# Kernel tuning notes

Measured on AMD Instinct MI355X. Metric: run time of the kernel, lower is better.

Reference implementation:

```python
import jax, jax.numpy as jnp
import numpy as np

B, N, H, P, R = 16, 256, 768, 2048, 3


def setup_inputs() -> dict:
    key = jax.random.key(0)
    ks = jax.random.split(key, 7)
    s_h = 1.0 / np.sqrt(H)
    s_p = 1.0 / np.sqrt(P)
    return {
        "features": jax.random.normal(ks[0], (B, N, H), dtype=jnp.float32),
        "head_W": jax.random.uniform(ks[1], (P, H), jnp.float32, -s_h, s_h),
        "head_b": jax.random.uniform(ks[2], (P,), jnp.float32, -s_h, s_h),
        "tail_W": jax.random.uniform(ks[3], (P, H), jnp.float32, -s_h, s_h),
        "tail_b": jax.random.uniform(ks[4], (P,), jnp.float32, -s_h, s_h),
        "bil_W": jax.random.uniform(ks[5], (R, P, P), jnp.float32, -s_p, s_p),
        "bil_b": jax.random.uniform(ks[6], (R,), jnp.float32, -s_p, s_p),
    }


def reference(features, head_W, head_b, tail_W, tail_b, bil_W, bil_b):
    # Linear projections (dropout is identity in eval mode)
    head = jnp.einsum("bnh,ph->bnp", features, head_W) + head_b  # [B,N,P]
    tail = jnp.einsum("bnh,ph->bnp", features, tail_W) + tail_b  # [B,N,P]
    # Bilinear over all region pairs, without materializing [B,N,N,P]:
    # first contract head with W[r] -> [B,N,R,P], then with tail -> [B,N,N,R]
    hw = jnp.einsum("bnp,rpq->bnrq", head, bil_W)                # [B,N,R,P]
    logits = jnp.einsum("bnrq,bmq->bnmr", hw, tail) + bil_b      # [B,N,N,R]
    return logits
```

## Files before the change

### kernel.cpp

```cpp
#include <hip/hip_runtime.h>

constexpr int Bb = 16;
constexpr int Nn = 256;
constexpr int Hh = 768;
constexpr int Pp = 2048;
constexpr int Rr = 3;
constexpr int Mm = Bb * Nn;
constexpr int HA = 896;
constexpr int KA = 2080;
constexpr int JA = Rr * HA;

typedef __bf16 bf16_t;
typedef __bf16 bf16x8 __attribute__((ext_vector_type(8)));
typedef __bf16 bf16x4 __attribute__((ext_vector_type(4)));
typedef float  floatx4 __attribute__((ext_vector_type(4)));

__device__ __forceinline__ void gld_lds16(const void* g, void* l) {
    __builtin_amdgcn_global_load_lds(
        (__attribute__((address_space(1))) void*)g,
        (__attribute__((address_space(3))) void*)l,
        16, 0, 0);
}

__global__ __launch_bounds__(256) void cvt_bilW(
    const float* __restrict__ in, bf16_t* __restrict__ out)
{
    const size_t i = (size_t)blockIdx.x * 256 + threadIdx.x;
    const float4 v0 = ((const float4*)in)[2 * i];
    const float4 v1 = ((const float4*)in)[2 * i + 1];
    bf16x8 o = { (bf16_t)v0.x, (bf16_t)v0.y, (bf16_t)v0.z, (bf16_t)v0.w,
                 (bf16_t)v1.x, (bf16_t)v1.y, (bf16_t)v1.z, (bf16_t)v1.w };
    ((bf16x8*)out)[i] = o;
}

__global__ __launch_bounds__(256) void build_Faug(
    const float* __restrict__ F, bf16_t* __restrict__ out)
{
    const int idx = blockIdx.x * 256 + threadIdx.x;
    const int n = idx / (HA / 4), c4 = idx % (HA / 4);
    const int h = c4 * 4;
    bf16x4 o;
    if (h < Hh) {
        float4 v = *(const float4*)(F + (size_t)n * Hh + h);
        o = { (bf16_t)v.x, (bf16_t)v.y, (bf16_t)v.z, (bf16_t)v.w };
    } else {
        #pragma unroll
        for (int e = 0; e < 4; ++e) o[e] = (bf16_t)((h + e == Hh) ? 1.0f : 0.0f);
    }
    *(bf16x4*)(out + (size_t)n * HA + h) = o;
}

__global__ __launch_bounds__(256) void build_tWaug(
    const float* __restrict__ tW, const float* __restrict__ bt,
    bf16_t* __restrict__ out)
{
    __shared__ float t[32][33];
    const int j0 = blockIdx.y * 32, q0 = blockIdx.x * 32;
    const int tx = threadIdx.x, ty = threadIdx.y;
    #pragma unroll
    for (int s = 0; s < 4; ++s) {
        const int q = q0 + ty + s * 8, j = j0 + tx;
        t[ty + s * 8][tx] = (j < Hh) ? tW[(size_t)q * Hh + j] : 0.0f;
    }
    __syncthreads();
    #pragma unroll
    for (int s = 0; s < 4; ++s) {
        const int j = j0 + ty + s * 8, q = q0 + tx;
        float v = t[tx][ty + s * 8];
        if (j == Hh) v = bt[q];
        else if (j > Hh) v = 0.0f;
        out[(size_t)j * Pp + q] = (bf16_t)v;
    }
}

__global__ __launch_bounds__(256) void build_hWaug(
    const float* __restrict__ hW, const float* __restrict__ bh,
    bf16_t* __restrict__ out)
{
    __shared__ float t[32][33];
    const int h0 = blockIdx.y * 32, p0 = blockIdx.x * 32;
    const int tx = threadIdx.x, ty = threadIdx.y;
    #pragma unroll
    for (int s = 0; s < 4; ++s) {
        const int p = p0 + ty + s * 8, h = h0 + tx;
        t[ty + s * 8][tx] = (p < Pp && h < Hh) ? hW[(size_t)p * Hh + h] : 0.0f;
    }
    __syncthreads();
    #pragma unroll
    for (int s = 0; s < 4; ++s) {
        const int h = h0 + ty + s * 8, p = p0 + tx;
        float v = t[tx][ty + s * 8];
        if (h == Hh) v = (p < Pp) ? bh[p] : (p == Pp ? 1.0f : 0.0f);
        else if (h > Hh) v = 0.0f;
        out[(size_t)h * KA + p] = (bf16_t)v;
    }
}

__global__ __launch_bounds__(256) void fill_T1cols(
    const float* __restrict__ bil_b, bf16_t* __restrict__ T1)
{
    const int idx = blockIdx.x * 256 + threadIdx.x;
    if (idx >= Rr * HA) return;
    const int r = idx / HA, j = idx % HA;
    bf16_t* p = T1 + (size_t)r * HA * KA + (size_t)j * KA + Pp;
    p[0] = (bf16_t)(j == Hh ? bil_b[r] : 0.0f);
    #pragma unroll
    for (int e = 1; e < 32; ++e) p[e] = (bf16_t)0.0f;
}

__global__ __launch_bounds__(256) void gemm_nt_128x64(
    const bf16_t* __restrict__ A, int lda,
    const bf16_t* __restrict__ B, int ldb, size_t sB,
    bf16_t* __restrict__ C, int ldc, size_t sC, int K)
{
    const int orig = blockIdx.y * 21 + blockIdx.x;
    const int wgid = (orig & 7) * 84 + (orig >> 3);
    const int n0 = (wgid / 21) * 64;
    const int mr = wgid % 21;
    const int m0 = (mr / 3) * 128;
    const int r  = mr % 3;
    B += (size_t)r * sB;
    C += (size_t)r * sC;

    __shared__ bf16_t As[2][128 * 32];
    __shared__ bf16_t Bs[2][64 * 32];

    const int tid = threadIdx.x;
    const int w = tid >> 6;
    const int l = tid & 63;

    const bf16_t* ga0 = A + (size_t)(m0 + (w << 4) + (l >> 2)) * lda + ((l & 3) << 3);
    const bf16_t* ga1 = ga0 + (size_t)64 * lda;
    const bf16_t* gb = B + (size_t)(n0 + (tid >> 2)) * ldb + ((tid & 3) << 3);

    const int wm = (w >> 1) << 6;
    const int wn = (w & 1) << 5;
    const int fr = l & 15;
    const int fq = (l >> 4) << 3;

    floatx4 acc[4][2] = {};

    {
        gld_lds16(ga0, (char*)As[0] + (w << 10));
        gld_lds16(ga1, (char*)As[0] + 4096 + (w << 10));
        gld_lds16(gb,  (char*)Bs[0] + (w << 10));
        ga0 += 32; ga1 += 32; gb += 32;
    }

    const int steps = K >> 5;
    for (int k = 0; k < steps; ++k) {
        __syncthreads();
        const int cur = k & 1;
        if (k + 1 < steps) {
            gld_lds16(ga0, (char*)As[cur ^ 1] + (w << 10));
            gld_lds16(ga1, (char*)As[cur ^ 1] + 4096 + (w << 10));
            gld_lds16(gb,  (char*)Bs[cur ^ 1] + (w << 10));
            ga0 += 32; ga1 += 32; gb += 32;
        }

        bf16x8 a[4], b[2];
        #pragma unroll
        for (int i = 0; i < 4; ++i)
            a[i] = *(const bf16x8*)&As[cur][(wm + i * 16 + fr) * 32 + fq];
        #pragma unroll
        for (int j = 0; j < 2; ++j)
            b[j] = *(const bf16x8*)&Bs[cur][(wn + j * 16 + fr) * 32 + fq];
        #pragma unroll
        for (int i = 0; i < 4; ++i)
            #pragma unroll
            for (int j = 0; j < 2; ++j)
                acc[i][j] = __builtin_amdgcn_mfma_f32_16x16x32_bf16(a[i], b[j], acc[i][j], 0, 0, 0);
    }

    const int em = m0 + wm + ((l >> 4) << 2);
    const int en = n0 + wn + (l & 15);
    #pragma unroll
    for (int i = 0; i < 4; ++i)
        #pragma unroll
        for (int j = 0; j < 2; ++j)
            #pragma unroll
            for (int rg = 0; rg < 4; ++rg)
                C[(size_t)(em + i * 16 + rg) * ldc + en + j * 16] = (bf16_t)acc[i][j][rg];
}

__global__ __launch_bounds__(256) void gemm_nt_64(
    const bf16_t* __restrict__ A, int lda, size_t sA,
    const bf16_t* __restrict__ B, int ldb, size_t sB,
    bf16_t* __restrict__ C, int ldc, size_t sC, int K)
{
    const int orig = (blockIdx.z * 14 + blockIdx.y) * 14 + blockIdx.x;
    const int xcd = orig & 7, idx = orig >> 3;
    const int wgid = (xcd < 4 ? xcd * 74 : 296 + (xcd - 4) * 73) + idx;
    const int r    = wgid / 196;
    const int rest = wgid % 196;
    const int m0 = (rest / 14) * 64;
    const int n0 = (rest % 14) * 64;
    A += (size_t)r * sA;
    B += (size_t)r * sB;
    C += (size_t)r * sC;

    __shared__ bf16_t As[2][64 * 32];
    __shared__ bf16_t Bs[2][64 * 32];

    const int tid = threadIdx.x;
    const int w = tid >> 6;
    const int l = tid & 63;

    const bf16_t* ga = A + (size_t)(m0 + (tid >> 2)) * lda + ((tid & 3) << 3);
    const bf16_t* gb = B + (size_t)(n0 + (tid >> 2)) * ldb + ((tid & 3) << 3);

    const int wm = (w >> 1) << 5;
    const int wn = (w & 1) << 5;
    const int fr = l & 15;
    const int fq = (l >> 4) << 3;

    floatx4 acc[2][2] = {};

    {
        gld_lds16(ga, (char*)As[0] + (w << 10));
        gld_lds16(gb, (char*)Bs[0] + (w << 10));
        ga += 32; gb += 32;
    }

    const int steps = K >> 5;
    for (int k = 0; k < steps; ++k) {
        __syncthreads();
        const int cur = k & 1;
        if (k + 1 < steps) {
            gld_lds16(ga, (char*)As[cur ^ 1] + (w << 10));
            gld_lds16(gb, (char*)Bs[cur ^ 1] + (w << 10));
            ga += 32; gb += 32;
        }

        bf16x8 a[2], b[2];
        #pragma unroll
        for (int i = 0; i < 2; ++i) {
            a[i] = *(const bf16x8*)&As[cur][(wm + i * 16 + fr) * 32 + fq];
            b[i] = *(const bf16x8*)&Bs[cur][(wn + i * 16 + fr) * 32 + fq];
        }
        #pragma unroll
        for (int i = 0; i < 2; ++i)
            #pragma unroll
            for (int j = 0; j < 2; ++j)
                acc[i][j] = __builtin_amdgcn_mfma_f32_16x16x32_bf16(a[i], b[j], acc[i][j], 0, 0, 0);
    }

    const int em = m0 + wm + ((l >> 4) << 2);
    const int en = n0 + wn + (l & 15);
    #pragma unroll
    for (int i = 0; i < 2; ++i)
        #pragma unroll
        for (int j = 0; j < 2; ++j)
            #pragma unroll
            for (int rg = 0; rg < 4; ++rg)
                C[(size_t)(em + i * 16 + rg) * ldc + en + j * 16] = (bf16_t)acc[i][j][rg];
}

__global__ __launch_bounds__(256) void gemm_nt_128(
    const bf16_t* __restrict__ A, int lda,
    const bf16_t* __restrict__ B, int ldb,
    bf16_t* __restrict__ C, int ldc, int K)
{
    const int orig = blockIdx.y * 21 + blockIdx.x;
    const int wgid = (orig & 7) * 84 + (orig >> 3);
    const int m0 = (wgid / 21) * 128;
    const int n0 = (wgid % 21) * 128;

    __shared__ bf16_t As[2][128 * 32];
    __shared__ bf16_t Bs[2][128 * 32];

    const int tid = threadIdx.x;
    const int w = tid >> 6;
    const int l = tid & 63;

    const int srow = (w << 4) + (l >> 2);
    const int scol = (l & 3) << 3;
    const bf16_t* ga0 = A + (size_t)(m0 + srow) * lda + scol;
    const bf16_t* ga1 = ga0 + (size_t)64 * lda;
    const bf16_t* gb0 = B + (size_t)(n0 + srow) * ldb + scol;
    const bf16_t* gb1 = gb0 + (size_t)64 * ldb;

    const int wm = (w >> 1) << 6;
    const int wn = (w & 1) << 6;
    const int fr = l & 15;
    const int fq = (l >> 4) << 3;

    floatx4 acc[4][4] = {};

    {
        char* a = (char*)As[0] + (w << 10);
        char* b = (char*)Bs[0] + (w << 10);
        gld_lds16(ga0, a); gld_lds16(ga1, a + 4096);
        gld_lds16(gb0, b); gld_lds16(gb1, b + 4096);
        ga0 += 32; ga1 += 32; gb0 += 32; gb1 += 32;
    }

    const int steps = K >> 5;
    for (int k = 0; k < steps; ++k) {
        __syncthreads();
        const int cur = k & 1;
        if (k + 1 < steps) {
            char* a = (char*)As[cur ^ 1] + (w << 10);
            char* b = (char*)Bs[cur ^ 1] + (w << 10);
            gld_lds16(ga0, a); gld_lds16(ga1, a + 4096);
            gld_lds16(gb0, b); gld_lds16(gb1, b + 4096);
            ga0 += 32; ga1 += 32; gb0 += 32; gb1 += 32;
        }

        bf16x8 a[4], b[4];
        #pragma unroll
        for (int i = 0; i < 4; ++i) {
            a[i] = *(const bf16x8*)&As[cur][(wm + i * 16 + fr) * 32 + fq];
            b[i] = *(const bf16x8*)&Bs[cur][(wn + i * 16 + fr) * 32 + fq];
        }
        #pragma unroll
        for (int i = 0; i < 4; ++i)
            #pragma unroll
            for (int j = 0; j < 4; ++j)
                acc[i][j] = __builtin_amdgcn_mfma_f32_16x16x32_bf16(a[i], b[j], acc[i][j], 0, 0, 0);
    }

    const int em = m0 + wm + ((l >> 4) << 2);
    const int en = n0 + wn + (l & 15);
    #pragma unroll
    for (int j = 0; j < 4; ++j) {
        const int n = en + j * 16;
        #pragma unroll
        for (int i = 0; i < 4; ++i) {
            #pragma unroll
            for (int rg = 0; rg < 4; ++rg)
                C[(size_t)(em + i * 16 + rg) * ldc + n] = (bf16_t)(acc[i][j][rg]);
        }
    }
}

__global__ __launch_bounds__(512) void gemm_out_fused(
    const bf16_t* __restrict__ FG,
    const bf16_t* __restrict__ FA,
    float* __restrict__ OUT)
{
    const int orig = (blockIdx.z * 4 + blockIdx.y) * 4 + blockIdx.x;
    const int wgid = (orig & 7) * 32 + (orig >> 3);
    const int b  = wgid >> 4;
    const int n0 = ((wgid >> 2) & 3) * 64;
    const int m0 = (wgid & 3) * 64;

    __shared__ bf16_t S[2][4][64 * 32];

    const int tid = threadIdx.x;
    const int w = tid >> 6;
    const int l = tid & 63;

    const int srow = ((w & 3) << 4) + (l >> 2);
    const int scol = (l & 3) << 3;
    const int t0 = w >> 2;
    const bf16_t* g0 = FG + (size_t)(b * Nn + n0 + srow) * JA + t0 * HA + scol;
    const bf16_t* g1 = (t0 == 0)
        ? FG + (size_t)(b * Nn + n0 + srow) * JA + 2 * HA + scol
        : FA + (size_t)(b * Nn + m0 + srow) * HA + scol;

    const int n_off = (w >> 2) << 5;
    const int m_off = (w & 3) << 4;
    const int fr = l & 15;
    const int fq = (l >> 4) << 3;

    floatx4 acc[Rr][2] = {};

    {
        char* base = (char*)&S[0][0][0];
        gld_lds16(g0, base + (w << 10));        g0 += 32;
        gld_lds16(g1, base + 8192 + (w << 10)); g1 += 32;
    }

    constexpr int STEPS = HA / 32;
    for (int k = 0; k < STEPS; ++k) {
        __syncthreads();
        const int cur = k & 1;
        if (k + 1 < STEPS) {
            char* base = (char*)&S[cur ^ 1][0][0];
            gld_lds16(g0, base + (w << 10));        g0 += 32;
            gld_lds16(g1, base + 8192 + (w << 10)); g1 += 32;
        }

        bf16x8 t = *(const bf16x8*)&S[cur][3][(m_off + fr) * 32 + fq];
        #pragma unroll
        for (int r = 0; r < Rr; ++r) {
            #pragma unroll
            for (int i = 0; i < 2; ++i) {
                bf16x8 a = *(const bf16x8*)&S[cur][r][(n_off + i * 16 + fr) * 32 + fq];
                acc[r][i] = __builtin_amdgcn_mfma_f32_16x16x32_bf16(a, t, acc[r][i], 0, 0, 0);
            }
        }
    }

    const int en_ = n0 + n_off + ((l >> 4) << 2);
    const int em_ = m0 + m_off + (l & 15);
    #pragma unroll
    for (int i = 0; i < 2; ++i)
        #pragma unroll
        for (int rg = 0; rg < 4; ++rg) {
            const int n = en_ + i * 16 + rg;
            float* o = OUT + (((size_t)b * Nn + n) * Nn + em_) * Rr;
            #pragma unroll
            for (int r = 0; r < Rr; ++r)
                o[r] = acc[r][i][rg];
        }
}

extern "C" void kernel_launch(void* const* d_in, const int* in_sizes, int n_in,
                              void* d_out, int out_size, void* d_ws, size_t ws_size,
                              hipStream_t stream) {
    const float* features = (const float*)d_in[0];
    const float* head_W   = (const float*)d_in[1];
    const float* head_b   = (const float*)d_in[2];
    const float* tail_W   = (const float*)d_in[3];
    const float* tail_b   = (const float*)d_in[4];
    const float* bil_W    = (const float*)d_in[5];
    const float* bil_b    = (const float*)d_in[6];
    float* out = (float*)d_out;

    char* ws = (char*)d_ws;
    bf16_t* Faug   = (bf16_t*)ws;  ws += (size_t)Mm * HA * 2;
    bf16_t* tWaug  = (bf16_t*)ws;  ws += (size_t)HA * Pp * 2;
    bf16_t* hWaug  = (bf16_t*)ws;  ws += (size_t)HA * KA * 2;
    bf16_t* T1taug = (bf16_t*)ws;  ws += (size_t)Rr * HA * KA * 2;
    char*   Z      = ws;
    bf16_t* bilWh  = (bf16_t*)Z;
    bf16_t* Bop    = (bf16_t*)Z;
    bf16_t* FG     = (bf16_t*)(Z + (size_t)Rr * HA * HA * 2);

    cvt_bilW<<<(Rr * Pp * Pp / 8) / 256, 256, 0, stream>>>(bil_W, bilWh);

    build_Faug<<<Mm * (HA / 4) / 256, 256, 0, stream>>>(features, Faug);
    build_tWaug<<<dim3(Pp / 32, HA / 32), dim3(32, 8), 0, stream>>>(tail_W, tail_b, tWaug);
    build_hWaug<<<dim3(KA / 32, HA / 32), dim3(32, 8), 0, stream>>>(head_W, head_b, hWaug);

    gemm_nt_128x64<<<dim3(21, 32), 256, 0, stream>>>(
        tWaug, Pp,
        bilWh, Pp, (size_t)Pp * Pp,
        T1taug, KA, (size_t)HA * KA, Pp);
    fill_T1cols<<<(Rr * HA + 255) / 256, 256, 0, stream>>>(bil_b, T1taug);

    gemm_nt_64<<<dim3(HA / 64, HA / 64, Rr), 256, 0, stream>>>(
        T1taug, KA, (size_t)HA * KA,
        hWaug, KA, 0,
        Bop, HA, (size_t)HA * HA, KA);

    gemm_nt_128<<<dim3(JA / 128, Mm / 128), 256, 0, stream>>>(
        Faug, HA,
        Bop, HA,
        FG, JA, HA);

    gemm_out_fused<<<dim3(Nn / 64, Nn / 64, Bb), 512, 0, stream>>>(FG, Faug, out);
}
```

Before: 242.0 us.

## Fuse three bilinear relations into one 512-thread GEMM tile sharing A loads

The T1 GEMM now computes all three relation outputs in one workgroup. Each block loads the A tile (tail weights) once and multiplies it against three B tiles, where before each relation was a separate block that reloaded A. The grid shrinks from 672 blocks of 256 threads to 224 blocks of 512 threads, with a new XCD-aware remapping. This cuts redundant A traffic but triples accumulator and LDS use per block and lowers the block count, which may hurt occupancy or load balance.

```diff
diff --git a/kernel.cpp b/kernel.cpp
--- a/kernel.cpp
+++ b/kernel.cpp
@@ -108,43 +108,41 @@
     for (int e = 1; e < 32; ++e) p[e] = (bf16_t)0.0f;
 }
 
-__global__ __launch_bounds__(256) void gemm_nt_128x64(
+__global__ __launch_bounds__(512) void gemm_nt3_128x64_w8(
     const bf16_t* __restrict__ A, int lda,
     const bf16_t* __restrict__ B, int ldb, size_t sB,
     bf16_t* __restrict__ C, int ldc, size_t sC, int K)
 {
-    const int orig = blockIdx.y * 21 + blockIdx.x;
-    const int wgid = (orig & 7) * 84 + (orig >> 3);
-    const int n0 = (wgid / 21) * 64;
-    const int mr = wgid % 21;
-    const int m0 = (mr / 3) * 128;
-    const int r  = mr % 3;
-    B += (size_t)r * sB;
-    C += (size_t)r * sC;
+    const int orig = blockIdx.x;
+    const int wgid = (orig & 7) * 28 + (orig >> 3);
+    const int n0 = (wgid / 7) * 64;
+    const int m0 = (wgid % 7) * 128;
 
     __shared__ bf16_t As[2][128 * 32];
-    __shared__ bf16_t Bs[2][64 * 32];
+    __shared__ bf16_t Bs[2][Rr * 64 * 32];
 
     const int tid = threadIdx.x;
     const int w = tid >> 6;
     const int l = tid & 63;
 
-    const bf16_t* ga0 = A + (size_t)(m0 + (w << 4) + (l >> 2)) * lda + ((l & 3) << 3);
-    const bf16_t* ga1 = ga0 + (size_t)64 * lda;
-    const bf16_t* gb = B + (size_t)(n0 + (tid >> 2)) * ldb + ((tid & 3) << 3);
-
-    const int wm = (w >> 1) << 6;
+    const bf16_t* ga = A + (size_t)(m0 + (w << 4) + (l >> 2)) * lda + ((l & 3) << 3);
+    const bf16_t* gb1 = B + (size_t)(w >> 2) * sB
+                      + (size_t)(n0 + ((w & 3) << 4) + (l >> 2)) * ldb + ((l & 3) << 3);
+    const bf16_t* gb2 = B + 2 * sB
+                      + (size_t)(n0 + (w << 4) + (l >> 2)) * ldb + ((l & 3) << 3);
+
+    const int wm = (w >> 1) << 5;
     const int wn = (w & 1) << 5;
     const int fr = l & 15;
     const int fq = (l >> 4) << 3;
 
-    floatx4 acc[4][2] = {};
+    floatx4 acc[Rr][2][2] = {};
 
     {
-        gld_lds16(ga0, (char*)As[0] + (w << 10));
-        gld_lds16(ga1, (char*)As[0] + 4096 + (w << 10));
-        gld_lds16(gb,  (char*)Bs[0] + (w << 10));
-        ga0 += 32; ga1 += 32; gb += 32;
+        gld_lds16(ga,  (char*)As[0] + (w << 10));
+        gld_lds16(gb1, (char*)Bs[0] + (w << 10));
+        if (w < 4) gld_lds16(gb2, (char*)Bs[0] + 8192 + (w << 10));
+        ga += 32; gb1 += 32; gb2 += 32;
     }
 
     const int steps = K >> 5;
@@ -152,35 +150,42 @@
         __syncthreads();
         const int cur = k & 1;
         if (k + 1 < steps) {
-            gld_lds16(ga0, (char*)As[cur ^ 1] + (w << 10));
-            gld_lds16(ga1, (char*)As[cur ^ 1] + 4096 + (w << 10));
-            gld_lds16(gb,  (char*)Bs[cur ^ 1] + (w << 10));
-            ga0 += 32; ga1 += 32; gb += 32;
-        }
-
-        bf16x8 a[4], b[2];
-        #pragma unroll
-        for (int i = 0; i < 4; ++i)
+            gld_lds16(ga,  (char*)As[cur ^ 1] + (w << 10));
+            gld_lds16(gb1, (char*)Bs[cur ^ 1] + (w << 10));
+            if (w < 4) gld_lds16(gb2, (char*)Bs[cur ^ 1] + 8192 + (w << 10));
+            ga += 32; gb1 += 32; gb2 += 32;
+        }
+
+        bf16x8 a[2];
+        #pragma unroll
+        for (int i = 0; i < 2; ++i)
             a[i] = *(const bf16x8*)&As[cur][(wm + i * 16 + fr) * 32 + fq];
         #pragma unroll
-        for (int j = 0; j < 2; ++j)
-            b[j] = *(const bf16x8*)&Bs[cur][(wn + j * 16 + fr) * 32 + fq];
-        #pragma unroll
-        for (int i = 0; i < 4; ++i)
+        for (int r = 0; r < Rr; ++r) {
+            bf16x8 b[2];
             #pragma unroll
             for (int j = 0; j < 2; ++j)
-                acc[i][j] = __builtin_amdgcn_mfma_f32_16x16x32_bf16(a[i], b[j], acc[i][j], 0, 0, 0);
+                b[j] = *(const bf16x8*)&Bs[cur][r * 2048 + (wn + j * 16 + fr) * 32 + fq];
+            #pragma unroll
+            for (int i = 0; i < 2; ++i)
+                #pragma unroll
+                for (int j = 0; j < 2; ++j)
+                    acc[r][i][j] = __builtin_amdgcn_mfma_f32_16x16x32_bf16(a[i], b[j], acc[r][i][j], 0, 0, 0);
+        }
     }
 
     const int em = m0 + wm + ((l >> 4) << 2);
     const int en = n0 + wn + (l & 15);
     #pragma unroll
-    for (int i = 0; i < 4; ++i)
-        #pragma unroll
-        for (int j = 0; j < 2; ++j)
-            #pragma unroll
-            for (int rg = 0; rg < 4; ++rg)
-                C[(size_t)(em + i * 16 + rg) * ldc + en + j * 16] = (bf16_t)acc[i][j][rg];
+    for (int r = 0; r < Rr; ++r)
+        #pragma unroll
+        for (int i = 0; i < 2; ++i)
+            #pragma unroll
+            for (int j = 0; j < 2; ++j)
+                #pragma unroll
+                for (int rg = 0; rg < 4; ++rg)
+                    C[(size_t)r * sC + (size_t)(em + i * 16 + rg) * ldc + en + j * 16]
+                        = (bf16_t)acc[r][i][j][rg];
 }
 
 __global__ __launch_bounds__(256) void gemm_nt_64(
@@ -435,7 +440,7 @@
     build_tWaug<<<dim3(Pp / 32, HA / 32), dim3(32, 8), 0, stream>>>(tail_W, tail_b, tWaug);
     build_hWaug<<<dim3(KA / 32, HA / 32), dim3(32, 8), 0, stream>>>(head_W, head_b, hWaug);
 
-    gemm_nt_128x64<<<dim3(21, 32), 256, 0, stream>>>(
+    gemm_nt3_128x64_w8<<<dim3(224), 512, 0, stream>>>(
         tWaug, Pp,
         bilWh, Pp, (size_t)Pp * Pp,
         T1taug, KA, (size_t)HA * KA, Pp);
```

New measurement: 249.5 us. 3.1% more time.
